# Performance work log

Measured on AMD Instinct MI355X. Metric: run time of the kernel, lower is better.

## Reference

```python
import jax, jax.numpy as jnp
import numpy as np
import math

DIM = 1024
NUM_HEADS = 16
HEAD_DIM = DIM // NUM_HEADS
BLOCK_SIZE = 64


def _block_mask(src_blocks, tgt_blocks, num_blocks):
    # Block-level BigBird mask: global first/last block columns, sliding window of 1, random blocks.
    i = jnp.arange(num_blocks)[:, None]
    j = jnp.arange(num_blocks)[None, :]
    band = jnp.abs(i - j) <= 1
    glob = (j == 0) | (j == num_blocks - 1)
    bm = band | glob
    bm = bm.at[src_blocks, tgt_blocks].set(True)
    return bm  # [nb, nb] bool


def setup_inputs() -> dict:
    key = jax.random.key(0)
    ks = jax.random.split(key, 12)
    B, S = 2, 2048
    x = jax.random.normal(ks[0], (B, S, DIM), dtype=jnp.float32)
    scale = 0.02
    Wq = jax.random.normal(ks[1], (DIM, DIM), dtype=jnp.float32) * scale
    bq = jnp.zeros((DIM,), dtype=jnp.float32)
    Wk = jax.random.normal(ks[2], (DIM, DIM), dtype=jnp.float32) * scale
    bk = jnp.zeros((DIM,), dtype=jnp.float32)
    Wv = jax.random.normal(ks[3], (DIM, DIM), dtype=jnp.float32) * scale
    bv = jnp.zeros((DIM,), dtype=jnp.float32)
    Wo = jax.random.normal(ks[4], (DIM, DIM), dtype=jnp.float32) * scale
    bo = jnp.zeros((DIM,), dtype=jnp.float32)
    num_blocks = S // BLOCK_SIZE
    src_blocks = jax.random.randint(ks[5], (3,), 0, num_blocks, dtype=jnp.int32)
    tgt_blocks = jax.random.randint(ks[6], (3,), 0, num_blocks, dtype=jnp.int32)
    return {"x": x, "Wq": Wq, "bq": bq, "Wk": Wk, "bk": bk, "Wv": Wv, "bv": bv,
            "Wo": Wo, "bo": bo, "src_blocks": src_blocks, "tgt_blocks": tgt_blocks}


def reference(x, Wq, bq, Wk, bk, Wv, bv, Wo, bo, src_blocks, tgt_blocks):
    B, S, _ = x.shape
    nb = S // BLOCK_SIZE
    # NOTE: original torch code uses .view (not transpose) to split heads; replicate faithfully.
    q = (x @ Wq.T + bq).reshape(B, NUM_HEADS, S, HEAD_DIM)
    k = (x @ Wk.T + bk).reshape(B, NUM_HEADS, S, HEAD_DIM)
    v = (x @ Wv.T + bv).reshape(B, NUM_HEADS, S, HEAD_DIM)
    bm = _block_mask(src_blocks, tgt_blocks, nb)
    mask = jnp.repeat(jnp.repeat(bm, BLOCK_SIZE, axis=0), BLOCK_SIZE, axis=1)  # [S, S]
    scores = jnp.einsum('bhqd,bhkd->bhqk', q, k) / math.sqrt(HEAD_DIM)
    scores = jnp.where(mask[None, None], scores, jnp.float32(-1e9))
    attn = jax.nn.softmax(scores, axis=-1)
    out = jnp.einsum('bhqk,bhkd->bhqd', attn, v)
    out = out.transpose(0, 2, 1, 3).reshape(B, S, DIM)
    return out @ Wo.T + bo
```

## Files before the change

### kernel.cpp

```cpp
#include <hip/hip_runtime.h>
#include <math.h>

typedef __attribute__((ext_vector_type(8))) short short8;
typedef __attribute__((ext_vector_type(4))) float f32x4;

#define SEQ 2048
#define NB  32

__device__ __forceinline__ unsigned short f2bf(float f) {
    unsigned u = __float_as_uint(f);
    u = (u + 0x7FFFu + ((u >> 16) & 1u)) >> 16;
    return (unsigned short)u;
}

__device__ __forceinline__ void gload16(const unsigned short* g, unsigned short* l) {
    __builtin_amdgcn_global_load_lds(
        (__attribute__((address_space(1))) void*)(void*)(g),
        (__attribute__((address_space(3))) void*)(l), 16, 0, 0);
}

__global__ __launch_bounds__(256) void cvt_all(const float* __restrict__ x,
                                               const float* __restrict__ w0,
                                               const float* __restrict__ w1,
                                               const float* __restrict__ w2,
                                               const float* __restrict__ w3,
                                               unsigned short* __restrict__ ox,
                                               unsigned short* __restrict__ o0,
                                               unsigned short* __restrict__ o1,
                                               unsigned short* __restrict__ o2,
                                               unsigned short* __restrict__ o3) {
    const int which = blockIdx.y;
    const float* in = (which == 0) ? x : (which == 1) ? w0 : (which == 2) ? w1
                       : (which == 3) ? w2 : w3;
    unsigned short* out = (which == 0) ? ox : (which == 1) ? o0 : (which == 2) ? o1
                          : (which == 3) ? o2 : o3;
    const int n8 = (which == 0) ? 524288 : 131072;
    int i = blockIdx.x * 256 + threadIdx.x;
    const int stride = gridDim.x * 256;
    for (; i < n8; i += stride) {
        const float4 a = ((const float4*)in)[i * 2];
        const float4 b = ((const float4*)in)[i * 2 + 1];
        uint4 o;
        o.x = f2bf(a.x) | ((unsigned)f2bf(a.y) << 16);
        o.y = f2bf(a.z) | ((unsigned)f2bf(a.w) << 16);
        o.z = f2bf(b.x) | ((unsigned)f2bf(b.y) << 16);
        o.w = f2bf(b.z) | ((unsigned)f2bf(b.w) << 16);
        ((uint4*)out)[i] = o;
    }
}

template <int BF16OUT, int BN>
__global__ __launch_bounds__(256) void gemm_bt(const unsigned short* __restrict__ A,
                                               const unsigned short* __restrict__ Wall,
                                               const float* __restrict__ b0,
                                               const float* __restrict__ b1,
                                               const float* __restrict__ b2,
                                               unsigned short* __restrict__ outb,
                                               float* __restrict__ outf) {
    constexpr int MI = (BN == 128) ? 4 : 2;
    constexpr int NI = 4;
    __shared__ __align__(16) unsigned short As[2][128 * 32];
    __shared__ __align__(16) unsigned short Bs[2][BN * 32];

    const int t = threadIdx.x;
    const int w = t >> 6, l = t & 63;
    const int bx = blockIdx.x;
    const int which = (BN == 128) ? (bx >> 3) : 0;
    const int n0 = (BN == 128) ? (bx & 7) * 128 : bx * 64;
    const int m0 = blockIdx.y * 128;
    const unsigned short* W = Wall + (size_t)which * (1024ull * 1024);
    const float* bias = (which == 0) ? b0 : (which == 1) ? b1 : b2;

    const int wr = (BN == 128) ? (w >> 1) * 64 : w * 32;
    const int wc = (BN == 128) ? (w & 1) * 64 : 0;

    f32x4 acc[MI][NI];
#pragma unroll
    for (int i = 0; i < MI; ++i)
#pragma unroll
        for (int j = 0; j < NI; ++j) acc[i][j] = f32x4{0.f, 0.f, 0.f, 0.f};

    const unsigned short* Ag = A + (size_t)(m0 + w * 32 + (l >> 2)) * 1024 + (l & 3) * 8;
    const unsigned short* Wg =
        W + (size_t)(n0 + ((BN == 128) ? w * 32 : w * 16) + (l >> 2)) * 1024 + (l & 3) * 8;

    auto STAGE = [&](unsigned short* Asb, unsigned short* Bsb, int k0) {
        gload16(Ag + k0, Asb + w * 1024);
        gload16(Ag + k0 + 16 * 1024, Asb + w * 1024 + 512);
        gload16(Wg + k0, Bsb + ((BN == 128) ? w * 1024 : w * 512));
        if (BN == 128) gload16(Wg + k0 + 16 * 1024, Bsb + w * 1024 + 512);
    };
    auto COMPUTE = [&](const unsigned short* Asb, const unsigned short* Bsb) {
        short8 af[MI], bfr[NI];
#pragma unroll
        for (int mi = 0; mi < MI; ++mi)
            af[mi] = *(const short8*)&Asb[(wr + mi * 16 + (l & 15)) * 32 + (l >> 4) * 8];
#pragma unroll
        for (int ni = 0; ni < NI; ++ni)
            bfr[ni] = *(const short8*)&Bsb[(wc + ni * 16 + (l & 15)) * 32 + (l >> 4) * 8];
#pragma unroll
        for (int mi = 0; mi < MI; ++mi)
#pragma unroll
            for (int ni = 0; ni < NI; ++ni)
                acc[mi][ni] = __builtin_amdgcn_mfma_f32_16x16x32_bf16(af[mi], bfr[ni],
                                                                      acc[mi][ni], 0, 0, 0);
    };
#define WAITV_INFLIGHT()                                                  \
    do {                                                                  \
        if constexpr (BN == 128)                                          \
            asm volatile("s_waitcnt vmcnt(4)" ::: "memory");              \
        else                                                              \
            asm volatile("s_waitcnt vmcnt(3)" ::: "memory");              \
        __builtin_amdgcn_sched_barrier(0);                                \
    } while (0)
#define BAR()                                                             \
    do {                                                                  \
        __builtin_amdgcn_s_barrier();                                     \
        __builtin_amdgcn_sched_barrier(0);                                \
    } while (0)
#define READS_DONE_BAR()                                                  \
    do {                                                                  \
        asm volatile("s_waitcnt lgkmcnt(0)" ::: "memory");                \
        __builtin_amdgcn_sched_barrier(0);                                \
        __builtin_amdgcn_s_barrier();                                     \
        __builtin_amdgcn_sched_barrier(0);                                \
    } while (0)

    STAGE(As[0], Bs[0], 0);
#pragma unroll 1
    for (int kt2 = 0; kt2 < 16; ++kt2) {
        STAGE(As[1], Bs[1], (kt2 * 2 + 1) * 32);
        WAITV_INFLIGHT();
        BAR();
        COMPUTE(As[0], Bs[0]);
        READS_DONE_BAR();

        if (kt2 < 15) {
            STAGE(As[0], Bs[0], (kt2 * 2 + 2) * 32);
            WAITV_INFLIGHT();
        } else {
            asm volatile("s_waitcnt vmcnt(0)" ::: "memory");
            __builtin_amdgcn_sched_barrier(0);
        }
        BAR();
        COMPUTE(As[1], Bs[1]);
        if (kt2 < 15) READS_DONE_BAR();
    }
#undef WAITV_INFLIGHT
#undef BAR
#undef READS_DONE_BAR

    const int g = l >> 4, c = l & 15;
#pragma unroll
    for (int ni = 0; ni < NI; ++ni) {
        const int n = n0 + wc + ni * 16 + c;
        const float bv = bias[n];
#pragma unroll
        for (int mi = 0; mi < MI; ++mi) {
#pragma unroll
            for (int j = 0; j < 4; ++j) {
                const size_t m = (size_t)(m0 + wr + mi * 16 + g * 4 + j);
                const float v = acc[mi][ni][j] + bv;
                if (BF16OUT)
                    (outb + (size_t)which * (4096ull * 1024))[m * 1024 + n] = f2bf(v);
                else
                    outf[m * 1024 + n] = v;
            }
        }
    }
}

__global__ __launch_bounds__(256) void attn_mfma(const unsigned short* __restrict__ qb_,
                                                 const unsigned short* __restrict__ kb_,
                                                 const unsigned short* __restrict__ vb_,
                                                 const int* __restrict__ srcb,
                                                 const int* __restrict__ tgtb,
                                                 unsigned short* __restrict__ outb) {
    __shared__ __align__(16) unsigned short Ks[64 * 72];
    __shared__ __align__(16) unsigned short Vs[64 * 72];
    __shared__ __align__(16) unsigned short Ps[4][16 * 72];

    const int t = threadIdx.x, w = t >> 6, l = t & 63;
    const int qi = blockIdx.x, h = blockIdx.y, b = blockIdx.z;
    const int g = l >> 4, c = l & 15;

    unsigned mask = 1u | (1u << (NB - 1)) | (1u << qi);
    if (qi > 0) mask |= 1u << (qi - 1);
    if (qi < NB - 1) mask |= 1u << (qi + 1);
#pragma unroll
    for (int tt = 0; tt < 3; ++tt)
        if (srcb[tt] == qi) mask |= 1u << (tgtb[tt] & 31);

    const size_t ho = (size_t)(b * 16 + h) * (SEQ * 64);
    const unsigned short* Q = qb_ + ho;
    const unsigned short* K = kb_ + ho;
    const unsigned short* V = vb_ + ho;

    short8 qf[2];
    {
        const unsigned short* qrow = Q + (size_t)(qi * 64 + w * 16 + c) * 64;
        qf[0] = *(const short8*)(qrow + g * 8);
        qf[1] = *(const short8*)(qrow + 32 + g * 8);
    }

    f32x4 oacc[4];
#pragma unroll
    for (int d = 0; d < 4; ++d) oacc[d] = f32x4{0.f, 0.f, 0.f, 0.f};
    float mrun = -INFINITY, lsum = 0.f;

    const int sr = t >> 2, sc = (t & 3) * 16;

    for (int kb = 0; kb < NB; ++kb) {
        if (!((mask >> kb) & 1u)) continue;

        const unsigned short* ksrc = K + (size_t)(kb * 64 + sr) * 64 + sc;
        const unsigned short* vsrc = V + (size_t)(kb * 64 + sr) * 64 + sc;
        uint4 k0 = *(const uint4*)ksrc, k1 = *(const uint4*)(ksrc + 8);
        uint4 v0 = *(const uint4*)vsrc, v1 = *(const uint4*)(vsrc + 8);

        __syncthreads();
        *(uint4*)&Ks[sr * 72 + sc] = k0;
        *(uint4*)&Ks[sr * 72 + sc + 8] = k1;
        {
            const unsigned short* p0 = (const unsigned short*)&v0;
            const unsigned short* p1 = (const unsigned short*)&v1;
#pragma unroll
            for (int e = 0; e < 8; ++e) {
                Vs[(sc + e) * 72 + sr] = p0[e];
                Vs[(sc + 8 + e) * 72 + sr] = p1[e];
            }
        }
        __syncthreads();

        f32x4 sacc[4];
#pragma unroll
        for (int kt = 0; kt < 4; ++kt) sacc[kt] = f32x4{0.f, 0.f, 0.f, 0.f};
#pragma unroll
        for (int kt = 0; kt < 4; ++kt) {
#pragma unroll
            for (int ks = 0; ks < 2; ++ks) {
                const short8 ka = *(const short8*)&Ks[(kt * 16 + c) * 72 + ks * 32 + g * 8];
                sacc[kt] = __builtin_amdgcn_mfma_f32_16x16x32_bf16(ka, qf[ks], sacc[kt], 0, 0, 0);
            }
        }

        float sv[16];
        float tmax = -INFINITY;
#pragma unroll
        for (int kt = 0; kt < 4; ++kt)
#pragma unroll
            for (int j = 0; j < 4; ++j) {
                const float x = sacc[kt][j] * 0.125f;
                sv[kt * 4 + j] = x;
                tmax = fmaxf(tmax, x);
            }
        tmax = fmaxf(tmax, __shfl_xor(tmax, 16));
        tmax = fmaxf(tmax, __shfl_xor(tmax, 32));
        const float newm = fmaxf(mrun, tmax);
        const float corr = __expf(mrun - newm);
        float ps = 0.f;
#pragma unroll
        for (int e = 0; e < 16; ++e) {
            const float p = __expf(sv[e] - newm);
            sv[e] = p;
            ps += p;
        }
        ps += __shfl_xor(ps, 16);
        ps += __shfl_xor(ps, 32);
        lsum = lsum * corr + ps;
        mrun = newm;
#pragma unroll
        for (int d = 0; d < 4; ++d)
#pragma unroll
            for (int j = 0; j < 4; ++j) oacc[d][j] *= corr;

        unsigned short* pw = &Ps[w][c * 72];
#pragma unroll
        for (int kt = 0; kt < 4; ++kt) {
            uint2 pk;
            pk.x = f2bf(sv[kt * 4 + 0]) | ((unsigned)f2bf(sv[kt * 4 + 1]) << 16);
            pk.y = f2bf(sv[kt * 4 + 2]) | ((unsigned)f2bf(sv[kt * 4 + 3]) << 16);
            *(uint2*)&pw[kt * 16 + g * 4] = pk;
        }
        asm volatile("s_waitcnt lgkmcnt(0)" ::: "memory");
        __builtin_amdgcn_sched_barrier(0);

#pragma unroll
        for (int ks = 0; ks < 2; ++ks) {
            const short8 pb = *(const short8*)&Ps[w][c * 72 + ks * 32 + g * 8];
#pragma unroll
            for (int dt = 0; dt < 4; ++dt) {
                const short8 va = *(const short8*)&Vs[(dt * 16 + c) * 72 + ks * 32 + g * 8];
                oacc[dt] = __builtin_amdgcn_mfma_f32_16x16x32_bf16(va, pb, oacc[dt], 0, 0, 0);
            }
        }
    }

    const float inv = 1.f / lsum;
    unsigned short* orow = outb + (size_t)(b * SEQ + qi * 64 + w * 16 + c) * 1024 + h * 64;
#pragma unroll
    for (int dt = 0; dt < 4; ++dt)
#pragma unroll
        for (int j = 0; j < 4; ++j)
            orow[dt * 16 + g * 4 + j] = f2bf(oacc[dt][j] * inv);
}

extern "C" void kernel_launch(void* const* d_in, const int* in_sizes, int n_in,
                              void* d_out, int out_size, void* d_ws, size_t ws_size,
                              hipStream_t stream) {
    const float* x  = (const float*)d_in[0];
    const float* Wq = (const float*)d_in[1];
    const float* bq = (const float*)d_in[2];
    const float* Wk = (const float*)d_in[3];
    const float* bk = (const float*)d_in[4];
    const float* Wv = (const float*)d_in[5];
    const float* bv = (const float*)d_in[6];
    const float* Wo = (const float*)d_in[7];
    const float* bo = (const float*)d_in[8];
    const int* srcb = (const int*)d_in[9];
    const int* tgtb = (const int*)d_in[10];

    unsigned short* wsu = (unsigned short*)d_ws;
    unsigned short* xbf   = wsu;
    unsigned short* wqkv  = wsu + 4194304ull;
    unsigned short* wobf  = wsu + 7340032ull;
    unsigned short* qkvbf = wsu + 8388608ull;
    unsigned short* attbf = wsu + 25165824ull;

    hipLaunchKernelGGL(cvt_all, dim3(512, 5), dim3(256), 0, stream,
                       x, Wq, Wk, Wv, Wo,
                       xbf, wqkv, wqkv + 1048576ull, wqkv + 2097152ull, wobf);

    hipLaunchKernelGGL((gemm_bt<1, 128>), dim3(24, 32), dim3(256), 0, stream,
                       xbf, wqkv, bq, bk, bv, qkvbf, (float*)nullptr);

    hipLaunchKernelGGL(attn_mfma, dim3(32, 16, 2), dim3(256), 0, stream,
                       qkvbf, qkvbf + 4194304ull, qkvbf + 2ull * 4194304ull,
                       srcb, tgtb, attbf);

    hipLaunchKernelGGL((gemm_bt<0, 64>), dim3(16, 32), dim3(256), 0, stream,
                       attbf, wobf, bo, bo, bo, (unsigned short*)nullptr, (float*)d_out);

    (void)in_sizes; (void)n_in; (void)out_size; (void)ws_size;
}
```

Measured before the change: 92.82 us.

## Shrink QKV GEMM M-tile to 64 and stage epilogue through LDS for coalesced stores

The QKV projection GEMM now uses a 64x128 tile instead of 128x128, doubling the grid to 1536 blocks so more blocks spread across the CUs. Both GEMMs also rewrite their epilogue to stage results in shared memory and write coalesced 16-byte vectors, replacing scattered 2-byte and 4-byte stores. The cost is more blocks re-reading the weights and extra LDS traffic and barriers in the epilogue.

```diff
diff --git a/kernel.cpp b/kernel.cpp
--- a/kernel.cpp
+++ b/kernel.cpp
@@ -49,7 +49,7 @@
     }
 }
 
-template <int BF16OUT, int BN>
+template <int BF16OUT, int BM, int BN>
 __global__ __launch_bounds__(256) void gemm_bt(const unsigned short* __restrict__ A,
                                                const unsigned short* __restrict__ Wall,
                                                const float* __restrict__ b0,
@@ -57,21 +57,24 @@
                                                const float* __restrict__ b2,
                                                unsigned short* __restrict__ outb,
                                                float* __restrict__ outf) {
-    constexpr int MI = (BN == 128) ? 4 : 2;
+    constexpr int MI = 2;
     constexpr int NI = 4;
-    __shared__ __align__(16) unsigned short As[2][128 * 32];
-    __shared__ __align__(16) unsigned short Bs[2][BN * 32];
+    __shared__ __align__(16) unsigned short SMEM[2 * BM * 32 + 2 * BN * 32];
+    unsigned short* As0 = SMEM;
+    unsigned short* As1 = SMEM + BM * 32;
+    unsigned short* Bs0 = SMEM + 2 * BM * 32;
+    unsigned short* Bs1 = SMEM + 2 * BM * 32 + BN * 32;
 
     const int t = threadIdx.x;
     const int w = t >> 6, l = t & 63;
     const int bx = blockIdx.x;
     const int which = (BN == 128) ? (bx >> 3) : 0;
     const int n0 = (BN == 128) ? (bx & 7) * 128 : bx * 64;
-    const int m0 = blockIdx.y * 128;
+    const int m0 = blockIdx.y * BM;
     const unsigned short* W = Wall + (size_t)which * (1024ull * 1024);
     const float* bias = (which == 0) ? b0 : (which == 1) ? b1 : b2;
 
-    const int wr = (BN == 128) ? (w >> 1) * 64 : w * 32;
+    const int wr = (BN == 128) ? (w >> 1) * 32 : w * 32;
     const int wc = (BN == 128) ? (w & 1) * 64 : 0;
 
     f32x4 acc[MI][NI];
@@ -80,15 +83,21 @@
 #pragma unroll
         for (int j = 0; j < NI; ++j) acc[i][j] = f32x4{0.f, 0.f, 0.f, 0.f};
 
-    const unsigned short* Ag = A + (size_t)(m0 + w * 32 + (l >> 2)) * 1024 + (l & 3) * 8;
-    const unsigned short* Wg =
-        W + (size_t)(n0 + ((BN == 128) ? w * 32 : w * 16) + (l >> 2)) * 1024 + (l & 3) * 8;
+    const unsigned short* Ag = A +
+        (size_t)(m0 + ((BN == 128) ? w * 16 : w * 32) + (l >> 2)) * 1024 + (l & 3) * 8;
+    const unsigned short* Wg = W +
+        (size_t)(n0 + ((BN == 128) ? w * 32 : w * 16) + (l >> 2)) * 1024 + (l & 3) * 8;
 
     auto STAGE = [&](unsigned short* Asb, unsigned short* Bsb, int k0) {
-        gload16(Ag + k0, Asb + w * 1024);
-        gload16(Ag + k0 + 16 * 1024, Asb + w * 1024 + 512);
-        gload16(Wg + k0, Bsb + ((BN == 128) ? w * 1024 : w * 512));
-        if (BN == 128) gload16(Wg + k0 + 16 * 1024, Bsb + w * 1024 + 512);
+        if constexpr (BN == 128) {
+            gload16(Ag + k0, Asb + w * 512);
+            gload16(Wg + k0, Bsb + w * 1024);
+            gload16(Wg + k0 + 16 * 1024, Bsb + w * 1024 + 512);
+        } else {
+            gload16(Ag + k0, Asb + w * 1024);
+            gload16(Ag + k0 + 16 * 1024, Asb + w * 1024 + 512);
+            gload16(Wg + k0, Bsb + w * 512);
+        }
     };
     auto COMPUTE = [&](const unsigned short* Asb, const unsigned short* Bsb) {
         short8 af[MI], bfr[NI];
@@ -107,10 +116,7 @@
     };
 #define WAITV_INFLIGHT()                                                  \
     do {                                                                  \
-        if constexpr (BN == 128)                                          \
-            asm volatile("s_waitcnt vmcnt(4)" ::: "memory");              \
-        else                                                              \
-            asm volatile("s_waitcnt vmcnt(3)" ::: "memory");              \
+        asm volatile("s_waitcnt vmcnt(3)" ::: "memory");                  \
         __builtin_amdgcn_sched_barrier(0);                                \
     } while (0)
 #define BAR()                                                             \
@@ -126,46 +132,74 @@
         __builtin_amdgcn_sched_barrier(0);                                \
     } while (0)
 
-    STAGE(As[0], Bs[0], 0);
+    STAGE(As0, Bs0, 0);
 #pragma unroll 1
     for (int kt2 = 0; kt2 < 16; ++kt2) {
-        STAGE(As[1], Bs[1], (kt2 * 2 + 1) * 32);
+        STAGE(As1, Bs1, (kt2 * 2 + 1) * 32);
         WAITV_INFLIGHT();
         BAR();
-        COMPUTE(As[0], Bs[0]);
+        COMPUTE(As0, Bs0);
         READS_DONE_BAR();
 
         if (kt2 < 15) {
-            STAGE(As[0], Bs[0], (kt2 * 2 + 2) * 32);
+            STAGE(As0, Bs0, (kt2 * 2 + 2) * 32);
             WAITV_INFLIGHT();
         } else {
             asm volatile("s_waitcnt vmcnt(0)" ::: "memory");
             __builtin_amdgcn_sched_barrier(0);
         }
         BAR();
-        COMPUTE(As[1], Bs[1]);
+        COMPUTE(As1, Bs1);
         if (kt2 < 15) READS_DONE_BAR();
     }
 #undef WAITV_INFLIGHT
 #undef BAR
 #undef READS_DONE_BAR
 
+    __syncthreads();
     const int g = l >> 4, c = l & 15;
-#pragma unroll
-    for (int ni = 0; ni < NI; ++ni) {
-        const int n = n0 + wc + ni * 16 + c;
-        const float bv = bias[n];
-#pragma unroll
+    if constexpr (BF16OUT) {
+        unsigned short* eb = SMEM + w * (32 * 72);
+#pragma unroll
+        for (int ni = 0; ni < NI; ++ni) {
+            const float bv = bias[n0 + wc + ni * 16 + c];
+#pragma unroll
+            for (int mi = 0; mi < MI; ++mi)
+#pragma unroll
+                for (int j = 0; j < 4; ++j)
+                    eb[(mi * 16 + g * 4 + j) * 72 + ni * 16 + c] =
+                        f2bf(acc[mi][ni][j] + bv);
+        }
+        asm volatile("s_waitcnt lgkmcnt(0)" ::: "memory");
+        __builtin_amdgcn_sched_barrier(0);
+        unsigned short* outw = outb + (size_t)which * (4096ull * 1024);
+        const int r1 = l >> 1, hh = (l & 1) * 32;
+        const unsigned short* src = eb + r1 * 72 + hh;
+        unsigned short* dst = &outw[(size_t)(m0 + wr + r1) * 1024 + n0 + wc + hh];
+#pragma unroll
+        for (int q = 0; q < 4; ++q)
+            *(uint4*)(dst + q * 8) = *(const uint4*)(src + q * 8);
+    } else {
+        float* ef = (float*)SMEM + w * (16 * 68);
+#pragma unroll 1
         for (int mi = 0; mi < MI; ++mi) {
 #pragma unroll
-            for (int j = 0; j < 4; ++j) {
-                const size_t m = (size_t)(m0 + wr + mi * 16 + g * 4 + j);
-                const float v = acc[mi][ni][j] + bv;
-                if (BF16OUT)
-                    (outb + (size_t)which * (4096ull * 1024))[m * 1024 + n] = f2bf(v);
-                else
-                    outf[m * 1024 + n] = v;
-            }
+            for (int ni = 0; ni < NI; ++ni) {
+                const float bv = bias[n0 + wc + ni * 16 + c];
+#pragma unroll
+                for (int j = 0; j < 4; ++j)
+                    ef[(g * 4 + j) * 68 + ni * 16 + c] = acc[mi][ni][j] + bv;
+            }
+            asm volatile("s_waitcnt lgkmcnt(0)" ::: "memory");
+            __builtin_amdgcn_sched_barrier(0);
+            const int r2 = l >> 2, qq = (l & 3) * 16;
+            const float* srcf = ef + r2 * 68 + qq;
+            float* dstf = &outf[(size_t)(m0 + wr + mi * 16 + r2) * 1024 + n0 + wc + qq];
+#pragma unroll
+            for (int q = 0; q < 4; ++q)
+                *(float4*)(dstf + q * 4) = *(const float4*)(srcf + q * 4);
+            asm volatile("s_waitcnt lgkmcnt(0)" ::: "memory");
+            __builtin_amdgcn_sched_barrier(0);
         }
     }
 }
@@ -331,14 +365,14 @@
                        x, Wq, Wk, Wv, Wo,
                        xbf, wqkv, wqkv + 1048576ull, wqkv + 2097152ull, wobf);
 
-    hipLaunchKernelGGL((gemm_bt<1, 128>), dim3(24, 32), dim3(256), 0, stream,
+    hipLaunchKernelGGL((gemm_bt<1, 64, 128>), dim3(24, 64), dim3(256), 0, stream,
                        xbf, wqkv, bq, bk, bv, qkvbf, (float*)nullptr);
 
     hipLaunchKernelGGL(attn_mfma, dim3(32, 16, 2), dim3(256), 0, stream,
                        qkvbf, qkvbf + 4194304ull, qkvbf + 2ull * 4194304ull,
                        srcb, tgtb, attbf);
 
-    hipLaunchKernelGGL((gemm_bt<0, 64>), dim3(16, 32), dim3(256), 0, stream,
+    hipLaunchKernelGGL((gemm_bt<0, 128, 64>), dim3(16, 32), dim3(256), 0, stream,
                        attbf, wobf, bo, bo, bo, (unsigned short*)nullptr, (float*)d_out);
 
     (void)in_sizes; (void)n_in; (void)out_size; (void)ws_size;
```

New measurement: 110.0 us. 18.5% more time.
